# Optimization experiments

Measured on AMD Instinct MI355X. Metric: run time of the kernel, lower is better.

Reference implementation:

```python
import jax, jax.numpy as jnp
import numpy as np

B, S = 16, 512
FRAME, D_MODEL, H = 438, 800, 8
DH = D_MODEL // H
FFN = 1024
HID, POSE = 1024, 274
WIN, COND, LAMB = 100, 10, 0.01


def setup_inputs() -> dict:
    key = jax.random.key(0)
    ks = jax.random.split(key, 16)
    rn = lambda k, shp: jax.random.normal(k, shp, jnp.float32) * 0.02
    return {
        'src_seq': jax.random.normal(ks[0], (B, S, FRAME), jnp.float32),
        'src_pos': jnp.tile(jnp.arange(1, S + 1, dtype=jnp.int32), (B, 1)),
        'tgt_seq': jax.random.normal(ks[1], (B, S, POSE), jnp.float32),
        'vec_h': jnp.zeros((B, HID), jnp.float32),
        'vec_c': jnp.zeros((B, HID), jnp.float32),
        'dec_output': jnp.zeros((B, POSE), jnp.float32),
        'emb_W': rn(ks[2], (FRAME, D_MODEL)), 'emb_b': jnp.zeros((D_MODEL,), jnp.float32),
        'pos_table': rn(ks[3], (S + 1, D_MODEL)),
        'Wq': rn(ks[4], (D_MODEL, D_MODEL)), 'Wk': rn(ks[5], (D_MODEL, D_MODEL)),
        'Wv': rn(ks[6], (D_MODEL, D_MODEL)), 'Wo': rn(ks[7], (D_MODEL, D_MODEL)),
        'ln1_g': jnp.ones((D_MODEL,), jnp.float32), 'ln1_b': jnp.zeros((D_MODEL,), jnp.float32),
        'ffn_W1': rn(ks[8], (D_MODEL, FFN)), 'ffn_b1': jnp.zeros((FFN,), jnp.float32),
        'ffn_W2': rn(ks[9], (FFN, D_MODEL)), 'ffn_b2': jnp.zeros((D_MODEL,), jnp.float32),
        'ln2_g': jnp.ones((D_MODEL,), jnp.float32), 'ln2_b': jnp.zeros((D_MODEL,), jnp.float32),
        'lstm_Wx': rn(ks[10], (POSE, 4 * HID)), 'lstm_Wh': rn(ks[11], (HID, 4 * HID)),
        'lstm_b': jnp.zeros((4 * HID,), jnp.float32),
        'out_W': rn(ks[12], (HID + D_MODEL, POSE)), 'out_b': jnp.zeros((POSE,), jnp.float32),
        'epoch_i': 100,
    }


def _ln(x, g, b):
    m = x.mean(-1, keepdims=True)
    v = ((x - m) ** 2).mean(-1, keepdims=True)
    return (x - m) * jax.lax.rsqrt(v + 1e-6) * g + b


def _encoder(src_seq, src_pos, emb_W, emb_b, pos_table, Wq, Wk, Wv, Wo,
             ln1_g, ln1_b, ffn_W1, ffn_b1, ffn_W2, ffn_b2, ln2_g, ln2_b):
    b, s, _ = src_seq.shape
    x = src_seq @ emb_W + emb_b + pos_table[src_pos]  # (B,S,D)
    q = (x @ Wq).reshape(b, s, H, DH)
    k = (x @ Wk).reshape(b, s, H, DH)
    v = (x @ Wv).reshape(b, s, H, DH)
    idx = jnp.arange(s)
    band = jnp.abs(idx[:, None] - idx[None, :]) <= WIN  # sliding-window mask
    scores = jnp.einsum('bqhd,bkhd->bhqk', q, k) / np.float32(np.sqrt(DH))
    scores = jnp.where(band[None, None], scores, jnp.float32(-1e9))
    attn = jax.nn.softmax(scores, axis=-1)
    o = jnp.einsum('bhqk,bkhd->bqhd', attn, v).reshape(b, s, D_MODEL)
    x = _ln(x + o @ Wo, ln1_g, ln1_b)
    h = jax.nn.relu(x @ ffn_W1 + ffn_b1) @ ffn_W2 + ffn_b2
    return _ln(x + h, ln2_g, ln2_b)


def _sched_mask(seq_len, epoch_i):
    p = int(epoch_i * LAMB)  # prediction steps per block (static int)
    pattern = np.concatenate([np.zeros(p, np.bool_), np.ones(COND, np.bool_)])
    return jnp.asarray(np.tile(pattern, seq_len)[:seq_len])


def reference(src_seq, src_pos, tgt_seq, vec_h, vec_c, dec_output,
              emb_W, emb_b, pos_table, Wq, Wk, Wv, Wo, ln1_g, ln1_b,
              ffn_W1, ffn_b1, ffn_W2, ffn_b2, ln2_g, ln2_b,
              lstm_Wx, lstm_Wh, lstm_b, out_W, out_b, epoch_i):
    enc = _encoder(src_seq, src_pos, emb_W, emb_b, pos_table, Wq, Wk, Wv, Wo,
                   ln1_g, ln1_b, ffn_W1, ffn_b1, ffn_W2, ffn_b2, ln2_g, ln2_b)
    seq_len = tgt_seq.shape[1]
    smask = _sched_mask(seq_len, epoch_i)

    def step(carry, xs):
        h, c, prev = carry
        tgt_t, enc_t, m = xs
        x = jnp.where(m, tgt_t, jax.lax.stop_gradient(prev))  # scheduled sampling
        gates = x @ lstm_Wx + h @ lstm_Wh + lstm_b
        i, f, g, o = jnp.split(gates, 4, axis=-1)  # torch LSTMCell gate order
        c = jax.nn.sigmoid(f) * c + jax.nn.sigmoid(i) * jnp.tanh(g)
        h = jax.nn.sigmoid(o) * jnp.tanh(c)
        out = jnp.concatenate([h, enc_t], axis=1) @ out_W + out_b
        return (h, c, out), out

    xs = (tgt_seq.transpose(1, 0, 2), enc.transpose(1, 0, 2), smask)
    _, outs = jax.lax.scan(step, (vec_h, vec_c, dec_output), xs)
    return outs.transpose(1, 0, 2)  # (B,S,POSE)
```

## Files before the change

### kernel.cpp

```cpp
#include <hip/hip_runtime.h>
#include <math.h>

#define B_ 16
#define S_ 512
#define FRAME_ 438
#define DM_ 800
#define H_ 8
#define DH_ 100
#define FFN_ 1024
#define HID_ 1024
#define POSE_ 274
#define WIN_ 100
#define G4_ 4096
#define KPA_ 1536
#define KPB_ 1024
#define NBLK_SCAN 512
#define WLS_ 1312
#define WLSZ_ (8 * WLS_ + 256)
#define NSLOT_ 64

#define RING_SLOT_F 16384L

__device__ __forceinline__ void st_coh(float* p, float v)
{
    asm volatile("global_store_dword %0, %1, off sc0 sc1"
                 :: "v"(p), "v"(v) : "memory");
}

__device__ __forceinline__ void st_coh_u32(unsigned* p, unsigned v)
{
    asm volatile("global_store_dword %0, %1, off sc0 sc1"
                 :: "v"(p), "v"(v) : "memory");
}

__device__ __forceinline__ unsigned ld_coh_u32(const unsigned* p)
{
    unsigned v;
    asm volatile("global_load_dword %0, %1, off sc0 sc1\n\t"
                 "s_waitcnt vmcnt(0)"
                 : "=v"(v) : "v"(p) : "memory");
    return v;
}

__host__ __device__ __forceinline__ float* ring_slot(float* R, int n)
{
    long off;
    if (n < 248)      off = 30539776L + (long)n * RING_SLOT_F;
    else if (n < 444) off = 4259840L + (long)(n - 248) * RING_SLOT_F;
    else              off = 2244608L + (long)(n - 444) * RING_SLOT_F;
    return R + off;
}

__global__ __launch_bounds__(256) void gemm128(
    const float* __restrict__ A, const float* __restrict__ Bm,
    float* __restrict__ C, int M, int N, int K,
    const float* __restrict__ bias, const float* __restrict__ res,
    const int* __restrict__ posidx, const float* __restrict__ postab,
    int relu)
{
    __shared__ float As[2][16 * 132];
    __shared__ float Bs[2][16 * 132];
    int m0 = blockIdx.x * 128, n0 = blockIdx.y * 128;
    int tid = threadIdx.x;
    int tx = tid & 15, ty = tid >> 4;
    float acc[8][8];
#pragma unroll
    for (int i = 0; i < 8; ++i)
#pragma unroll
        for (int j = 0; j < 8; ++j) acc[i][j] = 0.f;

    float ra[8], rb[8];
    auto loadA = [&](int k0) {
#pragma unroll
        for (int i = 0; i < 8; ++i) {
            int idx = i * 256 + tid;
            int m = idx >> 4, kl = idx & 15;
            int r = m0 + m, k = k0 + kl;
            ra[i] = (r < M && k < K) ? A[(long)r * K + k] : 0.f;
        }
    };
    auto loadB = [&](int k0) {
#pragma unroll
        for (int i = 0; i < 8; ++i) {
            int idx = i * 256 + tid;
            int n = idx & 127, k = idx >> 7;
            int kk = k0 + k, nn = n0 + n;
            rb[i] = (kk < K && nn < N) ? Bm[(long)kk * N + nn] : 0.f;
        }
    };

    loadA(0); loadB(0);
    int cur = 0;
    for (int k0 = 0; k0 < K; k0 += 16) {
#pragma unroll
        for (int i = 0; i < 8; ++i) {
            int idx = i * 256 + tid;
            As[cur][(idx & 15) * 132 + (idx >> 4)] = ra[i];
        }
#pragma unroll
        for (int i = 0; i < 8; ++i) {
            int idx = i * 256 + tid;
            Bs[cur][(idx >> 7) * 132 + (idx & 127)] = rb[i];
        }
        __syncthreads();
        if (k0 + 16 < K) { loadA(k0 + 16); loadB(k0 + 16); }
#pragma unroll
        for (int kk = 0; kk < 16; ++kk) {
            float4 a0 = *(const float4*)&As[cur][kk * 132 + ty * 4];
            float4 a1 = *(const float4*)&As[cur][kk * 132 + 64 + ty * 4];
            float4 b0 = *(const float4*)&Bs[cur][kk * 132 + tx * 4];
            float4 b1 = *(const float4*)&Bs[cur][kk * 132 + 64 + tx * 4];
            float a[8] = {a0.x, a0.y, a0.z, a0.w, a1.x, a1.y, a1.z, a1.w};
            float b[8] = {b0.x, b0.y, b0.z, b0.w, b1.x, b1.y, b1.z, b1.w};
#pragma unroll
            for (int i = 0; i < 8; ++i)
#pragma unroll
                for (int j = 0; j < 8; ++j) acc[i][j] += a[i] * b[j];
        }
        cur ^= 1;
    }
#pragma unroll
    for (int i = 0; i < 8; ++i) {
        int m = m0 + ((i < 4) ? (ty * 4 + i) : (64 + ty * 4 + i - 4));
        if (m >= M) continue;
#pragma unroll
        for (int j = 0; j < 8; ++j) {
            int n = n0 + ((j < 4) ? (tx * 4 + j) : (64 + tx * 4 + j - 4));
            if (n >= N) continue;
            float v = acc[i][j];
            if (bias) v += bias[n];
            if (res) v += res[(long)m * N + n];
            if (posidx) v += postab[(long)posidx[m] * N + n];
            if (relu) v = fmaxf(v, 0.f);
            C[(long)m * N + n] = v;
        }
    }
}

__global__ __launch_bounds__(256) void ln_f32(
    const float* __restrict__ X, float* __restrict__ Y,
    const float* __restrict__ g, const float* __restrict__ b, int N)
{
    int m = blockIdx.x;
    const float* x = X + (long)m * N;
    __shared__ float red[256];
    int tid = threadIdx.x;
    float s = 0.f;
    for (int i = tid; i < N; i += 256) s += x[i];
    red[tid] = s; __syncthreads();
    for (int o = 128; o > 0; o >>= 1) { if (tid < o) red[tid] += red[tid + o]; __syncthreads(); }
    float mean = red[0] / N;
    __syncthreads();
    float v = 0.f;
    for (int i = tid; i < N; i += 256) { float d = x[i] - mean; v += d * d; }
    red[tid] = v; __syncthreads();
    for (int o = 128; o > 0; o >>= 1) { if (tid < o) red[tid] += red[tid + o]; __syncthreads(); }
    float rs = rsqrtf(red[0] / N + 1e-6f);
    for (int i = tid; i < N; i += 256)
        Y[(long)m * N + i] = (x[i] - mean) * rs * g[i] + b[i];
}

__global__ __launch_bounds__(256) void attn_f32(
    const float* __restrict__ Q, const float* __restrict__ K,
    const float* __restrict__ V, float* __restrict__ O)
{
    int blk = blockIdx.x;
    int qt = blk & 127; int bh = blk >> 7;
    int h = bh & 7; int b = bh >> 3;
    int q0 = qt * 4;
    int tid = threadIdx.x;

    __shared__ float qv[4][DH_];
    __shared__ float sc[4][208];
    __shared__ float red[256];
    __shared__ float inv_den[4];

    for (int i = tid; i < 4 * DH_; i += 256) {
        int qi = i / DH_, d = i - qi * DH_;
        qv[qi][d] = Q[(long)(b * S_ + q0 + qi) * DM_ + h * DH_ + d];
    }
    __syncthreads();

    int w = tid;
    int k = q0 - WIN_ + w;
    bool kvalid = (w < 204) && (k >= 0) && (k < S_);
    float dots[4] = {0.f, 0.f, 0.f, 0.f};
    if (kvalid) {
        const float* krow = K + (long)(b * S_ + k) * DM_ + h * DH_;
        for (int d = 0; d < DH_; ++d) {
            float kvv = krow[d];
#pragma unroll
            for (int qi = 0; qi < 4; ++qi) dots[qi] += qv[qi][d] * kvv;
        }
    }
#pragma unroll
    for (int qi = 0; qi < 4; ++qi) {
        int wq = w - qi;
        if (w < 204 && wq >= 0 && wq < 201)
            sc[qi][wq] = kvalid ? dots[qi] * 0.1f : -1e30f;
    }
    __syncthreads();

    for (int qi = 0; qi < 4; ++qi) {
        float vmax = (tid < 201) ? sc[qi][tid] : -1e30f;
        red[tid] = vmax; __syncthreads();
        for (int o = 128; o > 0; o >>= 1) { if (tid < o) red[tid] = fmaxf(red[tid], red[tid + o]); __syncthreads(); }
        float mx = red[0];
        __syncthreads();
        float e = 0.f;
        if (tid < 201) { e = __expf(sc[qi][tid] - mx); sc[qi][tid] = e; }
        red[tid] = e; __syncthreads();
        for (int o = 128; o > 0; o >>= 1) { if (tid < o) red[tid] += red[tid + o]; __syncthreads(); }
        if (tid == 0) inv_den[qi] = 1.f / red[0];
        __syncthreads();
    }

    if (tid < DH_) {
        int d = tid;
        float o_[4] = {0.f, 0.f, 0.f, 0.f};
        for (int w2 = 0; w2 < 204; ++w2) {
            int k2 = q0 - WIN_ + w2;
            if (k2 < 0 || k2 >= S_) continue;
            float vv = V[(long)(b * S_ + k2) * DM_ + h * DH_ + d];
#pragma unroll
            for (int qi = 0; qi < 4; ++qi) {
                int wq = w2 - qi;
                if (wq >= 0 && wq < 201) o_[qi] += sc[qi][wq] * vv;
            }
        }
#pragma unroll
        for (int qi = 0; qi < 4; ++qi)
            O[(long)(b * S_ + q0 + qi) * DM_ + h * DH_ + d] = o_[qi] * inv_den[qi];
    }
}

__global__ __launch_bounds__(256) void g3_kernel(
    const float* __restrict__ outb, const float* __restrict__ Wx, float* __restrict__ g3)
{
    int j = blockIdx.x * 256 + threadIdx.x;
    if (j >= G4_) return;
    float s = 0.f;
    for (int p = 0; p < POSE_; ++p) s += outb[p] * Wx[(long)p * G4_ + j];
    g3[j] = s;
}

__global__ __launch_bounds__(256) void init_state(
    const float* __restrict__ vh, float* __restrict__ ring0,
    unsigned* __restrict__ bar)
{
    int i = blockIdx.x * 256 + threadIdx.x;
    if (i < B_ * HID_) {
        int bb = i >> 10, hid = i & 1023;
        ring0[hid * 16 + bb] = vh[i];
    }
    if (i < 4096) bar[i] = 0u;
}

__global__ __launch_bounds__(256) void xb_gather(
    const float* __restrict__ X, float* __restrict__ XB,
    const int* __restrict__ epoch)
{
    long idx = (long)blockIdx.x * 256 + threadIdx.x;
    int s = (int)(idx / 12800);
    int rem = (int)(idx - (long)s * 12800);
    int bb = rem / 800, k = rem - bb * 800;
    int p = (int)((double)epoch[0] * 0.01);
    float v = 0.f;
    if (p > 0) {
        int per = p + 10;
        int t = (s / p) * per + (s % p);
        if (t >= 1 && t < S_) v = X[((long)bb * S_ + (t - 1)) * DM_ + k];
    }
    XB[idx] = v;
}

__global__ __launch_bounds__(256) void tr_cat(
    const float* __restrict__ in1, const float* __restrict__ in2,
    float* __restrict__ WT, int K1, int K2, int KP)
{
    __shared__ float tile[64][65];
    int k0 = blockIdx.x * 64, c0 = blockIdx.y * 64;
    int tid = threadIdx.x;
    int cl = tid & 63, kr = tid >> 6;
#pragma unroll
    for (int i = 0; i < 16; ++i) {
        int kl = i * 4 + kr;
        int k = k0 + kl, c = c0 + cl;
        float v = 0.f;
        if (k < K1) v = in1[(long)k * G4_ + c];
        else if (k < K1 + K2) v = in2[(long)(k - K1) * G4_ + c];
        tile[kl][cl] = v;
    }
    __syncthreads();
    int kl2 = tid & 63, cr = tid >> 6;
#pragma unroll
    for (int i = 0; i < 16; ++i) {
        int ci = i * 4 + cr;
        WT[(long)(c0 + ci) * KP + k0 + kl2] = tile[kl2][ci];
    }
}

__global__ __launch_bounds__(256, 2) void lstm_scan(
    float* __restrict__ Rbase,
    const float* __restrict__ vec_c,
    const float* __restrict__ WT_A, const float* __restrict__ WT_Bh,
    const float* __restrict__ g3, const float* __restrict__ lstm_b,
    const int* __restrict__ epoch,
    const float* __restrict__ tgt, const float* __restrict__ dec0,
    const float* __restrict__ ENCB, float* __restrict__ Hall,
    unsigned* __restrict__ bar)
{
    __shared__ float WL[WLSZ_];
    __shared__ float panA[256 * 17];
    __shared__ float panB[256 * 17];
    float* red = panA;
    float* gst = panA + 2304;

    int tid = threadIdx.x;
    int hid0 = blockIdx.x * 2;
    int kq = tid >> 4, b = tid & 15;
    int b3 = tid >> 1, hh = tid & 1;
    int p = (int)((double)epoch[0] * 0.01);
    int per = p + 10;
    unsigned grp = (unsigned)blockIdx.x >> 4;
    unsigned* gcnt = bar;
    unsigned* root = bar + 1024;
    unsigned* genA = bar + 1056;

#pragma unroll
    for (int c = 0; c < 8; ++c) {
        const float* src = WT_A + (long)((c >> 1) * 1024 + hid0 + (c & 1)) * KPA_;
        for (int i = tid * 4; i < WLS_; i += 1024)
            *(float4*)&WL[c * WLS_ + i] = *(const float4*)&src[i];
    }
    for (int i = 8 * WLS_ + tid; i < WLSZ_; i += 256) WL[i] = 0.f;

    float c_reg = 0.f;
    if (tid < 32) c_reg = vec_c[b3 * HID_ + hid0 + hh];
    __syncthreads();

    for (int t = 0; t < S_; ++t) {
        bool msk = (t % per) >= p;
        bool useA = msk || (t == 0);
        const float* hrd = ring_slot(Rbase, t);
        float*       hwr = ring_slot(Rbase, t + 1);

        float acc[8]  = {0.f, 0.f, 0.f, 0.f, 0.f, 0.f, 0.f, 0.f};
        float acc2[8] = {0.f, 0.f, 0.f, 0.f, 0.f, 0.f, 0.f, 0.f};

        auto fma_wl = [&](int P, float* a, const float* pn) {
            int kb = P + kq * 16;
#pragma unroll
            for (int j4 = 0; j4 < 4; ++j4) {
                float4 w[8];
#pragma unroll
                for (int c = 0; c < 8; ++c)
                    w[c] = *(const float4*)&WL[c * WLS_ + kb + j4 * 4];
                float h0 = pn[(kq * 16 + j4 * 4 + 0) * 17 + b];
                float h1 = pn[(kq * 16 + j4 * 4 + 1) * 17 + b];
                float h2 = pn[(kq * 16 + j4 * 4 + 2) * 17 + b];
                float h3 = pn[(kq * 16 + j4 * 4 + 3) * 17 + b];
#pragma unroll
                for (int c = 0; c < 8; ++c)
                    a[c] += w[c].x * h0 + w[c].y * h1 + w[c].z * h2 + w[c].w * h3;
            }
        };
        auto loadh4 = [&](float4 v[4], int P) {
            const float* q = hrd + (long)(P + tid) * 16;
            v[0] = *(const float4*)(q);      v[1] = *(const float4*)(q + 4);
            v[2] = *(const float4*)(q + 8);  v[3] = *(const float4*)(q + 12);
        };
        auto writecol = [&](const float4 v[4], float* pn) {
            float* pp = &pn[tid * 17];
            pp[0]=v[0].x;  pp[1]=v[0].y;  pp[2]=v[0].z;  pp[3]=v[0].w;
            pp[4]=v[1].x;  pp[5]=v[1].y;  pp[6]=v[1].z;  pp[7]=v[1].w;
            pp[8]=v[2].x;  pp[9]=v[2].y;  pp[10]=v[2].z; pp[11]=v[2].w;
            pp[12]=v[3].x; pp[13]=v[3].y; pp[14]=v[3].z; pp[15]=v[3].w;
        };

        float tp4[16], tp5[16];
        if (useA) {
#pragma unroll
            for (int bb = 0; bb < 16; ++bb) {
                const float* src = msk ? &tgt[((long)bb * S_ + t) * POSE_]
                                       : &dec0[(long)bb * POSE_];
                tp4[bb] = src[tid];
                tp5[bb] = (tid < POSE_ - 256) ? src[256 + tid] : 0.f;
            }
        }

        if (useA) {
#pragma unroll
            for (int bb = 0; bb < 16; ++bb) panA[tid * 17 + bb] = tp4[bb];
            __syncthreads();
#pragma unroll
            for (int bb = 0; bb < 16; ++bb) panB[tid * 17 + bb] = tp5[bb];
            fma_wl(1024, acc2, panA);
            __syncthreads();
            fma_wl(1280, acc2, panB);
        }

        if (t > 0) {
            if (tid == 0)
                while (ld_coh_u32(&genA[grp * 32]) < (unsigned)t)
                    __builtin_amdgcn_s_sleep(2);
            __syncthreads();
        }

        float4 hA[4], hB[4], hC[4], hD[4];
        loadh4(hA, 0); loadh4(hB, 256); loadh4(hC, 512); loadh4(hD, 768);
        if (useA) {
            writecol(hA, panA); __syncthreads();
            writecol(hB, panB); fma_wl(0, acc, panA);   __syncthreads();
            writecol(hC, panA); fma_wl(256, acc, panB); __syncthreads();
            writecol(hD, panB); fma_wl(512, acc, panA); __syncthreads();
            fma_wl(768, acc, panB); __syncthreads();
        } else {
            const float* wrow[8];
#pragma unroll
            for (int c = 0; c < 8; ++c)
                wrow[c] = WT_Bh + (long)((c >> 1) * 1024 + hid0 + (c & 1)) * KPB_;
            auto fmaB = [&](int P, const float* pn) {
                int kb = P + kq * 16;
#pragma unroll
                for (int j4 = 0; j4 < 4; ++j4) {
                    float4 w[8];
#pragma unroll
                    for (int c = 0; c < 8; ++c)
                        w[c] = *(const float4*)(wrow[c] + kb + j4 * 4);
                    float h0 = pn[(kq * 16 + j4 * 4 + 0) * 17 + b];
                    float h1 = pn[(kq * 16 + j4 * 4 + 1) * 17 + b];
                    float h2 = pn[(kq * 16 + j4 * 4 + 2) * 17 + b];
                    float h3 = pn[(kq * 16 + j4 * 4 + 3) * 17 + b];
#pragma unroll
                    for (int c = 0; c < 8; ++c)
                        acc[c] += w[c].x * h0 + w[c].y * h1 + w[c].z * h2 + w[c].w * h3;
                }
            };
            writecol(hA, panA); __syncthreads();
            writecol(hB, panB); fmaB(0, panA);   __syncthreads();
            writecol(hC, panA); fmaB(256, panB); __syncthreads();
            writecol(hD, panB); fmaB(512, panA); __syncthreads();
            fmaB(768, panB); __syncthreads();
        }

#pragma unroll
        for (int c = 0; c < 8; ++c) red[(b * 16 + kq) * 9 + c] = acc[c] + acc2[c];
        __syncthreads();

        if (tid < 128) {
            int ob = tid >> 3, oc = tid & 7;
            float s = 0.f;
#pragma unroll
            for (int q = 0; q < 16; ++q) s += red[(ob * 16 + q) * 9 + oc];
            int gcol = (oc >> 1) * 1024 + hid0 + (oc & 1);
            s += lstm_b[gcol];
            if (!useA) {
                int sidx = ((t / per) * p + (t % per)) & (NSLOT_ - 1);
                s += g3[gcol] + ENCB[((long)(sidx * 16 + ob)) * G4_ + gcol];
            }
            gst[oc * 16 + ob] = s;
        }
        __syncthreads();

        if (tid < 32) {
            int hid = hid0 + hh;
            float iv = gst[(0 * 2 + hh) * 16 + b3];
            float fv = gst[(1 * 2 + hh) * 16 + b3];
            float gv = gst[(2 * 2 + hh) * 16 + b3];
            float ov = gst[(3 * 2 + hh) * 16 + b3];
            float ig = 1.f / (1.f + __expf(-iv));
            float fg = 1.f / (1.f + __expf(-fv));
            float og = 1.f / (1.f + __expf(-ov));
            float cn = fg * c_reg + ig * tanhf(gv);
            float hn = og * tanhf(cn);
            c_reg = cn;
            st_coh(&hwr[hid * 16 + b3], hn);
            Hall[((long)b3 * S_ + t) * HID_ + hid] = hn;
        }

        if (tid == 0) {
            asm volatile("s_waitcnt vmcnt(0)" ::: "memory");
            unsigned tk = __hip_atomic_fetch_add(&gcnt[grp * 32], 1u,
                              __ATOMIC_RELAXED, __HIP_MEMORY_SCOPE_AGENT);
            if (tk == (unsigned)(16 * t + 15)) {
                unsigned r = __hip_atomic_fetch_add(root, 1u,
                                 __ATOMIC_RELAXED, __HIP_MEMORY_SCOPE_AGENT);
                if (r == (unsigned)(32 * t + 31)) {
#pragma unroll
                    for (int j = 0; j < 32; ++j)
                        st_coh_u32(&genA[j * 32], (unsigned)(t + 1));
                }
            }
        }
        __syncthreads();
    }
}

extern "C" void kernel_launch(void* const* d_in, const int* in_sizes, int n_in,
                              void* d_out, int out_size, void* d_ws, size_t ws_size,
                              hipStream_t stream) {
    const float* src_seq  = (const float*)d_in[0];
    const int*   src_pos  = (const int*)  d_in[1];
    const float* tgt_seq  = (const float*)d_in[2];
    const float* vec_h    = (const float*)d_in[3];
    const float* vec_c    = (const float*)d_in[4];
    const float* dec0     = (const float*)d_in[5];
    const float* emb_W    = (const float*)d_in[6];
    const float* emb_b    = (const float*)d_in[7];
    const float* pos_tab  = (const float*)d_in[8];
    const float* Wq       = (const float*)d_in[9];
    const float* Wk       = (const float*)d_in[10];
    const float* Wv       = (const float*)d_in[11];
    const float* Wo       = (const float*)d_in[12];
    const float* ln1_g    = (const float*)d_in[13];
    const float* ln1_b    = (const float*)d_in[14];
    const float* ffn_W1   = (const float*)d_in[15];
    const float* ffn_b1   = (const float*)d_in[16];
    const float* ffn_W2   = (const float*)d_in[17];
    const float* ffn_b2   = (const float*)d_in[18];
    const float* ln2_g    = (const float*)d_in[19];
    const float* ln2_b    = (const float*)d_in[20];
    const float* lstm_Wx  = (const float*)d_in[21];
    const float* lstm_Wh  = (const float*)d_in[22];
    const float* lstm_b   = (const float*)d_in[23];
    const float* out_W    = (const float*)d_in[24];
    const float* out_b    = (const float*)d_in[25];
    const int*   epoch    = (const int*)  d_in[26];

    float* ws = (float*)d_ws;
    const long NX = (long)B_ * S_ * DM_;
    float* X      = ws;
    float* R      = X + NX;
    float* Qb     = R;
    float* Kb     = Qb + NX;
    float* Vb     = Kb + NX;
    float* Ob     = Vb + NX;
    float* FFNH   = Ob + NX;
    float* WEFF_t = R;
    float* G2m    = R + 4194304;
    float* WT_A   = R + 7471104;
    float* WT_B   = R + 13762560;
    float* ENCB   = R + 17956864;
    float* Hall   = R + 22151168;
    float* T1     = WEFF_t;
    float* XB     = R + 3375104;
    float* TAIL   = R + 34603008;
    float* G3v    = TAIL;
    unsigned* BAR = (unsigned*)G2m;

    const int M = B_ * S_;
    dim3 blk(256);

    gemm128<<<dim3(M / 128, (DM_ + 127) / 128), blk, 0, stream>>>(
        src_seq, emb_W, X, M, DM_, FRAME_, emb_b, nullptr, src_pos, pos_tab, 0);
    gemm128<<<dim3(M / 128, (DM_ + 127) / 128), blk, 0, stream>>>(
        X, Wq, Qb, M, DM_, DM_, nullptr, nullptr, nullptr, nullptr, 0);
    gemm128<<<dim3(M / 128, (DM_ + 127) / 128), blk, 0, stream>>>(
        X, Wk, Kb, M, DM_, DM_, nullptr, nullptr, nullptr, nullptr, 0);
    gemm128<<<dim3(M / 128, (DM_ + 127) / 128), blk, 0, stream>>>(
        X, Wv, Vb, M, DM_, DM_, nullptr, nullptr, nullptr, nullptr, 0);
    attn_f32<<<dim3(B_ * H_ * (S_ / 4)), blk, 0, stream>>>(Qb, Kb, Vb, Ob);
    gemm128<<<dim3(M / 128, (DM_ + 127) / 128), blk, 0, stream>>>(
        Ob, Wo, FFNH, M, DM_, DM_, nullptr, X, nullptr, nullptr, 0);
    ln_f32<<<dim3(M), blk, 0, stream>>>(FFNH, X, ln1_g, ln1_b, DM_);
    gemm128<<<dim3(M / 128, FFN_ / 128), blk, 0, stream>>>(
        X, ffn_W1, FFNH, M, FFN_, DM_, ffn_b1, nullptr, nullptr, nullptr, 1);
    gemm128<<<dim3(M / 128, (DM_ + 127) / 128), blk, 0, stream>>>(
        FFNH, ffn_W2, Ob, M, DM_, FFN_, ffn_b2, X, nullptr, nullptr, 0);
    ln_f32<<<dim3(M), blk, 0, stream>>>(Ob, X, ln2_g, ln2_b, DM_);

    gemm128<<<dim3(HID_ / 128, G4_ / 128), blk, 0, stream>>>(
        out_W, lstm_Wx, WEFF_t, HID_, G4_, POSE_, nullptr, lstm_Wh, nullptr, nullptr, 0);
    gemm128<<<dim3((DM_ + 127) / 128, G4_ / 128), blk, 0, stream>>>(
        out_W + (long)HID_ * POSE_, lstm_Wx, G2m, DM_, G4_, POSE_,
        nullptr, nullptr, nullptr, nullptr, 0);
    tr_cat<<<dim3(KPA_ / 64, G4_ / 64), blk, 0, stream>>>(
        lstm_Wh, lstm_Wx, WT_A, HID_, POSE_, KPA_);
    tr_cat<<<dim3(KPB_ / 64, G4_ / 64), blk, 0, stream>>>(
        WEFF_t, WEFF_t, WT_B, HID_, 0, KPB_);
    xb_gather<<<dim3(NSLOT_ * 16 * 800 / 256), blk, 0, stream>>>(X, XB, epoch);
    g3_kernel<<<dim3(G4_ / 256), blk, 0, stream>>>(out_b, lstm_Wx, G3v);
    gemm128<<<dim3(NSLOT_ * 16 / 128, G4_ / 128), blk, 0, stream>>>(
        XB, G2m, ENCB, NSLOT_ * 16, G4_, DM_, nullptr, nullptr, nullptr, nullptr, 0);
    init_state<<<dim3((B_ * HID_ + 255) / 256), blk, 0, stream>>>(
        vec_h, ring_slot(R, 0), BAR);
    gemm128<<<dim3(M / 128, (POSE_ + 127) / 128), blk, 0, stream>>>(
        X, out_W + (long)HID_ * POSE_, T1, M, POSE_, DM_, out_b,
        nullptr, nullptr, nullptr, 0);

    lstm_scan<<<dim3(NBLK_SCAN), blk, 0, stream>>>(
        R, vec_c, WT_A, WT_B, G3v, lstm_b, epoch,
        tgt_seq, dec0, ENCB, Hall, BAR);

    gemm128<<<dim3(M / 128, (POSE_ + 127) / 128), blk, 0, stream>>>(
        Hall, out_W, (float*)d_out, M, POSE_, HID_, nullptr, T1,
        nullptr, nullptr, 0);
}
```

Before: 9.582 ms.

## Store LSTM hidden ring batch-major and load operands into registers directly

The hidden-state ring changes from hid-major [hid][batch] to batch-major [batch][hid]. Each thread can then load its own contiguous 16-element k-slice of h (and of the target pose input) straight from global memory into registers. This removes the shared-memory transpose panels and the chain of __syncthreads between panel phases, and also drops the trailing barrier per timestep. The cost is more per-thread vector loads from global/L2 and more registers (16 float4 for h). Writes of h become scattered, two adjacent floats per batch row.

```diff
diff --git a/kernel.cpp b/kernel.cpp
--- a/kernel.cpp
+++ b/kernel.cpp
@@ -249,10 +249,7 @@
     unsigned* __restrict__ bar)
 {
     int i = blockIdx.x * 256 + threadIdx.x;
-    if (i < B_ * HID_) {
-        int bb = i >> 10, hid = i & 1023;
-        ring0[hid * 16 + bb] = vh[i];
-    }
+    if (i < B_ * HID_) ring0[i] = vh[i];
     if (i < 4096) bar[i] = 0u;
 }
 
@@ -311,10 +308,8 @@
     unsigned* __restrict__ bar)
 {
     __shared__ float WL[WLSZ_];
-    __shared__ float panA[256 * 17];
-    __shared__ float panB[256 * 17];
-    float* red = panA;
-    float* gst = panA + 2304;
+    __shared__ float red[2304];
+    __shared__ float gst[128];
 
     int tid = threadIdx.x;
     int hid0 = blockIdx.x * 2;
@@ -348,56 +343,41 @@
         float acc[8]  = {0.f, 0.f, 0.f, 0.f, 0.f, 0.f, 0.f, 0.f};
         float acc2[8] = {0.f, 0.f, 0.f, 0.f, 0.f, 0.f, 0.f, 0.f};
 
-        auto fma_wl = [&](int P, float* a, const float* pn) {
-            int kb = P + kq * 16;
+        if (useA) {
+            const float* src = msk ? &tgt[((long)b * S_ + t) * POSE_]
+                                   : &dec0[(long)b * POSE_];
+            float4 tr4[4];
+            float  tv[16];
+#pragma unroll
+            for (int j4 = 0; j4 < 4; ++j4)
+                tr4[j4] = *(const float4*)(src + kq * 16 + j4 * 4);
+#pragma unroll
+            for (int j = 0; j < 16; ++j) {
+                int kk = 256 + kq * 16 + j;
+                tv[j] = (kk < POSE_) ? src[kk] : 0.f;
+            }
 #pragma unroll
             for (int j4 = 0; j4 < 4; ++j4) {
                 float4 w[8];
 #pragma unroll
                 for (int c = 0; c < 8; ++c)
-                    w[c] = *(const float4*)&WL[c * WLS_ + kb + j4 * 4];
-                float h0 = pn[(kq * 16 + j4 * 4 + 0) * 17 + b];
-                float h1 = pn[(kq * 16 + j4 * 4 + 1) * 17 + b];
-                float h2 = pn[(kq * 16 + j4 * 4 + 2) * 17 + b];
-                float h3 = pn[(kq * 16 + j4 * 4 + 3) * 17 + b];
+                    w[c] = *(const float4*)&WL[c * WLS_ + 1024 + kq * 16 + j4 * 4];
+                float4 h4 = tr4[j4];
 #pragma unroll
                 for (int c = 0; c < 8; ++c)
-                    a[c] += w[c].x * h0 + w[c].y * h1 + w[c].z * h2 + w[c].w * h3;
-            }
-        };
-        auto loadh4 = [&](float4 v[4], int P) {
-            const float* q = hrd + (long)(P + tid) * 16;
-            v[0] = *(const float4*)(q);      v[1] = *(const float4*)(q + 4);
-            v[2] = *(const float4*)(q + 8);  v[3] = *(const float4*)(q + 12);
-        };
-        auto writecol = [&](const float4 v[4], float* pn) {
-            float* pp = &pn[tid * 17];
-            pp[0]=v[0].x;  pp[1]=v[0].y;  pp[2]=v[0].z;  pp[3]=v[0].w;
-            pp[4]=v[1].x;  pp[5]=v[1].y;  pp[6]=v[1].z;  pp[7]=v[1].w;
-            pp[8]=v[2].x;  pp[9]=v[2].y;  pp[10]=v[2].z; pp[11]=v[2].w;
-            pp[12]=v[3].x; pp[13]=v[3].y; pp[14]=v[3].z; pp[15]=v[3].w;
-        };
-
-        float tp4[16], tp5[16];
-        if (useA) {
-#pragma unroll
-            for (int bb = 0; bb < 16; ++bb) {
-                const float* src = msk ? &tgt[((long)bb * S_ + t) * POSE_]
-                                       : &dec0[(long)bb * POSE_];
-                tp4[bb] = src[tid];
-                tp5[bb] = (tid < POSE_ - 256) ? src[256 + tid] : 0.f;
-            }
-        }
-
-        if (useA) {
-#pragma unroll
-            for (int bb = 0; bb < 16; ++bb) panA[tid * 17 + bb] = tp4[bb];
-            __syncthreads();
-#pragma unroll
-            for (int bb = 0; bb < 16; ++bb) panB[tid * 17 + bb] = tp5[bb];
-            fma_wl(1024, acc2, panA);
-            __syncthreads();
-            fma_wl(1280, acc2, panB);
+                    acc2[c] += w[c].x * h4.x + w[c].y * h4.y + w[c].z * h4.z + w[c].w * h4.w;
+            }
+#pragma unroll
+            for (int j4 = 0; j4 < 4; ++j4) {
+                float4 w[8];
+#pragma unroll
+                for (int c = 0; c < 8; ++c)
+                    w[c] = *(const float4*)&WL[c * WLS_ + 1280 + kq * 16 + j4 * 4];
+#pragma unroll
+                for (int c = 0; c < 8; ++c)
+                    acc2[c] += w[c].x * tv[j4 * 4 + 0] + w[c].y * tv[j4 * 4 + 1]
+                             + w[c].z * tv[j4 * 4 + 2] + w[c].w * tv[j4 * 4 + 3];
+            }
         }
 
         if (t > 0) {
@@ -407,41 +387,54 @@
             __syncthreads();
         }
 
-        float4 hA[4], hB[4], hC[4], hD[4];
-        loadh4(hA, 0); loadh4(hB, 256); loadh4(hC, 512); loadh4(hD, 768);
+        float4 hr[16];
+        {
+            const float* hb = hrd + (long)b * HID_;
+#pragma unroll
+            for (int ph = 0; ph < 4; ++ph) {
+                const float* q = hb + ph * 256 + kq * 16;
+                hr[ph * 4 + 0] = *(const float4*)(q);
+                hr[ph * 4 + 1] = *(const float4*)(q + 4);
+                hr[ph * 4 + 2] = *(const float4*)(q + 8);
+                hr[ph * 4 + 3] = *(const float4*)(q + 12);
+            }
+        }
         if (useA) {
-            writecol(hA, panA); __syncthreads();
-            writecol(hB, panB); fma_wl(0, acc, panA);   __syncthreads();
-            writecol(hC, panA); fma_wl(256, acc, panB); __syncthreads();
-            writecol(hD, panB); fma_wl(512, acc, panA); __syncthreads();
-            fma_wl(768, acc, panB); __syncthreads();
+#pragma unroll
+            for (int ph = 0; ph < 4; ++ph) {
+                int kb = ph * 256 + kq * 16;
+#pragma unroll
+                for (int j4 = 0; j4 < 4; ++j4) {
+                    float4 w[8];
+#pragma unroll
+                    for (int c = 0; c < 8; ++c)
+                        w[c] = *(const float4*)&WL[c * WLS_ + kb + j4 * 4];
+                    float4 h4 = hr[ph * 4 + j4];
+#pragma unroll
+                    for (int c = 0; c < 8; ++c)
+                        acc[c] += w[c].x * h4.x + w[c].y * h4.y + w[c].z * h4.z + w[c].w * h4.w;
+                }
+            }
         } else {
             const float* wrow[8];
 #pragma unroll
             for (int c = 0; c < 8; ++c)
                 wrow[c] = WT_Bh + (long)((c >> 1) * 1024 + hid0 + (c & 1)) * KPB_;
-            auto fmaB = [&](int P, const float* pn) {
-                int kb = P + kq * 16;
+#pragma unroll
+            for (int ph = 0; ph < 4; ++ph) {
+                int kb = ph * 256 + kq * 16;
 #pragma unroll
                 for (int j4 = 0; j4 < 4; ++j4) {
                     float4 w[8];
 #pragma unroll
                     for (int c = 0; c < 8; ++c)
                         w[c] = *(const float4*)(wrow[c] + kb + j4 * 4);
-                    float h0 = pn[(kq * 16 + j4 * 4 + 0) * 17 + b];
-                    float h1 = pn[(kq * 16 + j4 * 4 + 1) * 17 + b];
-                    float h2 = pn[(kq * 16 + j4 * 4 + 2) * 17 + b];
-                    float h3 = pn[(kq * 16 + j4 * 4 + 3) * 17 + b];
+                    float4 h4 = hr[ph * 4 + j4];
 #pragma unroll
                     for (int c = 0; c < 8; ++c)
-                        acc[c] += w[c].x * h0 + w[c].y * h1 + w[c].z * h2 + w[c].w * h3;
+                        acc[c] += w[c].x * h4.x + w[c].y * h4.y + w[c].z * h4.z + w[c].w * h4.w;
                 }
-            };
-            writecol(hA, panA); __syncthreads();
-            writecol(hB, panB); fmaB(0, panA);   __syncthreads();
-            writecol(hC, panA); fmaB(256, panB); __syncthreads();
-            writecol(hD, panB); fmaB(512, panA); __syncthreads();
-            fmaB(768, panB); __syncthreads();
+            }
         }
 
 #pragma unroll
@@ -475,7 +468,7 @@
             float cn = fg * c_reg + ig * tanhf(gv);
             float hn = og * tanhf(cn);
             c_reg = cn;
-            st_coh(&hwr[hid * 16 + b3], hn);
+            st_coh(&hwr[(long)b3 * HID_ + hid], hn);
             Hall[((long)b3 * S_ + t) * HID_ + hid] = hn;
         }
 
@@ -493,7 +486,6 @@
                 }
             }
         }
-        __syncthreads();
     }
 }
 
```

After: 8.982 ms. 1.07x faster.
